# Performance work log

Hardware: AMD Instinct MI355X
Metric: run time of the kernel (lower is better)

## Reference

```python
import jax, jax.numpy as jnp
import numpy as np

NU, NM, D, E = 100000, 20000, 128, 1000000


def _seg_mean(feats, idx, n):
    # scatter-mean: zero for nodes with no incoming edges (PyG semantics)
    s = jax.ops.segment_sum(feats, idx, num_segments=n)
    c = jax.ops.segment_sum(jnp.ones((idx.shape[0], 1), feats.dtype), idx, num_segments=n)
    return s / jnp.maximum(c, 1.0)


def _hetero_sage(xu, xm, e_src, e_dst, Wl_um, Wr_um, b_um, Wl_mu, Wr_mu, b_mu):
    # ('user','rates','movie'): aggregate user features at movies
    agg_m = _seg_mean(xu[e_src], e_dst, xm.shape[0])          # [Nm, D]
    out_m = agg_m @ Wl_um + b_um + xm @ Wr_um                  # [Nm, H]
    # ('movie','rev_rates','user'): aggregate movie features at users
    agg_u = _seg_mean(xm[e_dst], e_src, xu.shape[0])          # [Nu, D]
    out_u = agg_u @ Wl_mu + b_mu + xu @ Wr_mu                  # [Nu, H]
    return out_u, out_m


def setup_inputs() -> dict:
    key = jax.random.key(0)
    ks = jax.random.split(key, 20)
    glorot = lambda k: (jax.random.normal(k, (D, D), jnp.float32) / np.sqrt(D)).astype(jnp.float32)
    inp = {
        "x_user": jax.random.normal(ks[0], (NU, D), jnp.float32),
        "x_movie": jax.random.normal(ks[1], (NM, D), jnp.float32),
        "edge_src": jax.random.randint(ks[2], (E,), 0, NU),
        "edge_dst": jax.random.randint(ks[3], (E,), 0, NM),
    }
    names = ["Wl1_um", "Wr1_um", "Wl1_mu", "Wr1_mu", "Wl2_um", "Wr2_um", "Wl2_mu", "Wr2_mu"]
    for i, n in enumerate(names):
        inp[n] = glorot(ks[4 + i])
    inp["b1_um"] = jnp.zeros((D,), jnp.float32)
    inp["b1_mu"] = jnp.zeros((D,), jnp.float32)
    inp["b2_um"] = jnp.zeros((D,), jnp.float32)
    inp["b2_mu"] = jnp.zeros((D,), jnp.float32)
    return inp


def reference(x_user, x_movie, Wl1_um, Wr1_um, Wl1_mu, Wr1_mu, Wl2_um, Wr2_um, Wl2_mu, Wr2_mu, b1_um, b1_mu, b2_um, b2_mu, edge_src, edge_dst):
    # layer 1 + relu (dropout = identity in eval) + residual
    h1_u, h1_m = _hetero_sage(x_user, x_movie, edge_src, edge_dst,
                              Wl1_um, Wr1_um, b1_um, Wl1_mu, Wr1_mu, b1_mu)
    r_u = x_user + jax.nn.relu(h1_u)
    r_m = x_movie + jax.nn.relu(h1_m)
    # layer 2 (dropout = identity in eval)
    out_u, out_m = _hetero_sage(r_u, r_m, edge_src, edge_dst,
                                Wl2_um, Wr2_um, b2_um, Wl2_mu, Wr2_mu, b2_mu)
    return out_u, out_m
```

## Files before the change

### kernel.cpp

```cpp
#include <hip/hip_runtime.h>
#include <stdint.h>

typedef unsigned short u16;
typedef unsigned int u32;
typedef __attribute__((ext_vector_type(8))) short short8;
typedef __attribute__((ext_vector_type(4))) float f32x4;
typedef __attribute__((ext_vector_type(4))) u32 u32x4;

__device__ __forceinline__ u16 f2bf(float f) {
    u32 x = __float_as_uint(f);
    u32 r = x + 0x7FFFu + ((x >> 16) & 1u);
    return (u16)(r >> 16);
}
__device__ __forceinline__ u32 pack2bf(float a, float b) {
    return (u32)f2bf(a) | ((u32)f2bf(b) << 16);
}
__device__ __forceinline__ float bflo(u32 w) { return __uint_as_float(w << 16); }
__device__ __forceinline__ float bfhi(u32 w) { return __uint_as_float(w & 0xFFFF0000u); }

struct WPtrs {
    const float* wl[4];
    const float* wr[4];
    u16* wout[4];
};

__global__ __launch_bounds__(256)
void prep_kernel(const int* __restrict__ src, const int* __restrict__ dst,
                 int* __restrict__ cnt, int* __restrict__ ranku,
                 int* __restrict__ rankm, int E, int nu, int nm,
                 const float* __restrict__ xu, const float* __restrict__ xm,
                 u32* __restrict__ xub, u32* __restrict__ xmb,
                 int eg4, int cg, WPtrs wp) {
    const int bid = blockIdx.x;
    const int tid = threadIdx.x;
    if (bid < eg4) {
        const int e0 = bid * 1024 + tid;
        int sv[4], dv[4];
        bool ok[4];
#pragma unroll
        for (int k = 0; k < 4; ++k) {
            int e = e0 + k * 256;
            ok[k] = (e < E);
            if (ok[k]) { sv[k] = src[e]; dv[k] = dst[e]; }
        }
#pragma unroll
        for (int k = 0; k < 4; ++k) {
            int e = e0 + k * 256;
            if (ok[k]) {
                if ((unsigned)sv[k] < (unsigned)nu &&
                    (unsigned)dv[k] < (unsigned)nm) {
                    ranku[e] = atomicAdd(&cnt[sv[k]], 1);
                    rankm[e] = atomicAdd(&cnt[nu + dv[k]], 1);
                } else {
                    ranku[e] = -1;
                }
            }
        }
    } else if (bid < eg4 + cg) {
        const int id = (bid - eg4) * 1024 + tid * 4;
        const int nuc = nu * 64;
        const int tot = nuc + nm * 64;
        if (id < tot) {
            const float* fin;
            u32* fout;
            int rel;
            if (id < nuc) { fin = xu; fout = xub; rel = id; }
            else          { fin = xm; fout = xmb; rel = id - nuc; }
            float4 p0 = ((const float4*)fin)[(rel >> 1)];
            float4 p1 = ((const float4*)fin)[(rel >> 1) + 1];
            u32x4 o = { pack2bf(p0.x, p0.y), pack2bf(p0.z, p0.w),
                        pack2bf(p1.x, p1.y), pack2bf(p1.z, p1.w) };
            *(u32x4*)(fout + rel) = o;
        }
    } else {
        const int unit = (bid - eg4 - cg) * 4 + (tid >> 6);
        if (unit < 256) {
            const int stack = unit >> 6, r = unit & 63, t = r >> 3, s = r & 7;
            const int lane = tid & 63;
            const float* Wl = wp.wl[stack];
            const float* Wr = wp.wr[stack];
            u16* outw = wp.wout[stack];
            const int n = t * 16 + (lane & 15);
            const int k0 = s * 32 + (lane >> 4) * 8;
            u16 v[8];
#pragma unroll
            for (int j = 0; j < 8; ++j) {
                int k = k0 + j;
                float f = (k < 128) ? Wl[k * 128 + n] : Wr[(k - 128) * 128 + n];
                v[j] = f2bf(f);
            }
            *(short8*)(outw + ((size_t)(t * 8 + s) * 64 + lane) * 8) = *(short8*)v;
        }
    }
}

__global__ __launch_bounds__(256)
void scan_partial(const int* __restrict__ cnt, int* __restrict__ bsum, int n) {
    __shared__ int s[256];
    const int tid = threadIdx.x;
    int base = blockIdx.x * 4096 + tid * 16;
    int sum = 0;
#pragma unroll
    for (int k = 0; k < 16; ++k) {
        int i = base + k;
        if (i < n) sum += cnt[i];
    }
    s[tid] = sum;
    __syncthreads();
    for (int d = 128; d > 0; d >>= 1) {
        if (tid < d) s[tid] += s[tid + d];
        __syncthreads();
    }
    if (tid == 0) bsum[blockIdx.x] = s[0];
}

__global__ __launch_bounds__(256)
void scan_apply(const int* __restrict__ cnt, const int* __restrict__ bsum,
                int* __restrict__ off, int n, int nb) {
    __shared__ int s[256];
    __shared__ int sb[64];
    __shared__ int pfx;
    const int tid = threadIdx.x;
    int base = blockIdx.x * 4096 + tid * 16;
    int v[16];
    int sum = 0;
#pragma unroll
    for (int k = 0; k < 16; ++k) {
        int i = base + k;
        v[k] = (i < n) ? cnt[i] : 0;
        sum += v[k];
    }
    s[tid] = sum;
    if (tid < 64) sb[tid] = (tid < nb) ? bsum[tid] : 0;
    __syncthreads();
    for (int d = 1; d < 256; d <<= 1) {
        int t = (tid >= d) ? s[tid - d] : 0;
        __syncthreads();
        s[tid] += t;
        __syncthreads();
    }
    if (tid == 0) {
        int p = 0;
        for (int b2 = 0; b2 < (int)blockIdx.x; ++b2) p += sb[b2];
        pfx = p;
        if ((int)blockIdx.x == nb - 1) off[n] = p + s[255];
    }
    __syncthreads();
    int run = pfx + s[tid] - sum;
#pragma unroll
    for (int k = 0; k < 16; ++k) {
        int i = base + k;
        if (i < n) off[i] = run;
        run += v[k];
    }
}

__global__ __launch_bounds__(256)
void fill_pos(const int* __restrict__ src, const int* __restrict__ dst,
              const int* __restrict__ ranku, const int* __restrict__ rankm,
              const int* __restrict__ off, int* __restrict__ nbr,
              int E, int nu) {
    const int e0 = blockIdx.x * 1024 + threadIdx.x;
    int sv[4], dv[4], ru[4], rm[4];
#pragma unroll
    for (int k = 0; k < 4; ++k) {
        int e = e0 + k * 256;
        ru[k] = -1;
        if (e < E) {
            ru[k] = ranku[e];
            sv[k] = src[e]; dv[k] = dst[e]; rm[k] = rankm[e];
        }
    }
#pragma unroll
    for (int k = 0; k < 4; ++k) {
        if (ru[k] >= 0) {
            nbr[off[sv[k]] + ru[k]] = dv[k];
            nbr[off[nu + dv[k]] + rm[k]] = sv[k];
        }
    }
}

template <int L1>
__device__ __forceinline__ void fused_body(
    const u32* __restrict__ featb, const float* __restrict__ xf,
    const u32* __restrict__ xb, const int* __restrict__ off,
    const int* __restrict__ nbr, const u16* __restrict__ wt,
    const float* __restrict__ bias, void* __restrict__ outp, int N, int blk) {
    __shared__ u32 sVb[16][132];
    const int tid = threadIdx.x;
    const int lane = tid & 63;
    const int wave = tid >> 6;
    const int base = blk * 16;
    const int q = lane >> 4;
    const int cl = lane & 15;

    for (int c = 0; c < 8; ++c) {
        const int i = wave * 8 + c;
        const int n = base + i;
        if (n < N) {
            const int b = off[n], e = off[n + 1];
            float a0 = 0.f, a1 = 0.f, a2 = 0.f, a3 = 0.f;
            float a4 = 0.f, a5 = 0.f, a6 = 0.f, a7 = 0.f;
            int t = b;
            for (; t + 15 < e; t += 16) {
                int g0 = nbr[t + q];
                int g1 = nbr[t + 4 + q];
                int g2 = nbr[t + 8 + q];
                int g3 = nbr[t + 12 + q];
                u32x4 v0 = *(const u32x4*)(featb + (size_t)g0 * 64 + cl * 4);
                u32x4 v1 = *(const u32x4*)(featb + (size_t)g1 * 64 + cl * 4);
                u32x4 v2 = *(const u32x4*)(featb + (size_t)g2 * 64 + cl * 4);
                u32x4 v3 = *(const u32x4*)(featb + (size_t)g3 * 64 + cl * 4);
                a0 += bflo(v0.x); a1 += bfhi(v0.x); a2 += bflo(v0.y); a3 += bfhi(v0.y);
                a4 += bflo(v0.z); a5 += bfhi(v0.z); a6 += bflo(v0.w); a7 += bfhi(v0.w);
                a0 += bflo(v1.x); a1 += bfhi(v1.x); a2 += bflo(v1.y); a3 += bfhi(v1.y);
                a4 += bflo(v1.z); a5 += bfhi(v1.z); a6 += bflo(v1.w); a7 += bfhi(v1.w);
                a0 += bflo(v2.x); a1 += bfhi(v2.x); a2 += bflo(v2.y); a3 += bfhi(v2.y);
                a4 += bflo(v2.z); a5 += bfhi(v2.z); a6 += bflo(v2.w); a7 += bfhi(v2.w);
                a0 += bflo(v3.x); a1 += bfhi(v3.x); a2 += bflo(v3.y); a3 += bfhi(v3.y);
                a4 += bflo(v3.z); a5 += bfhi(v3.z); a6 += bflo(v3.w); a7 += bfhi(v3.w);
            }
            for (; t < e; t += 4) {
                int it = t + q;
                if (it < e) {
                    u32x4 v = *(const u32x4*)(featb + (size_t)nbr[it] * 64 + cl * 4);
                    a0 += bflo(v.x); a1 += bfhi(v.x); a2 += bflo(v.y); a3 += bfhi(v.y);
                    a4 += bflo(v.z); a5 += bfhi(v.z); a6 += bflo(v.w); a7 += bfhi(v.w);
                }
            }
            a0 += __shfl_xor(a0, 16); a0 += __shfl_xor(a0, 32);
            a1 += __shfl_xor(a1, 16); a1 += __shfl_xor(a1, 32);
            a2 += __shfl_xor(a2, 16); a2 += __shfl_xor(a2, 32);
            a3 += __shfl_xor(a3, 16); a3 += __shfl_xor(a3, 32);
            a4 += __shfl_xor(a4, 16); a4 += __shfl_xor(a4, 32);
            a5 += __shfl_xor(a5, 16); a5 += __shfl_xor(a5, 32);
            a6 += __shfl_xor(a6, 16); a6 += __shfl_xor(a6, 32);
            a7 += __shfl_xor(a7, 16); a7 += __shfl_xor(a7, 32);
            const int dg = e - b;
            const float inv = 1.0f / (float)(dg > 1 ? dg : 1);
            if (q == 0) {
                u32x4 o = { pack2bf(a0 * inv, a1 * inv), pack2bf(a2 * inv, a3 * inv),
                            pack2bf(a4 * inv, a5 * inv), pack2bf(a6 * inv, a7 * inv) };
                *(u32x4*)&sVb[i][cl * 4] = o;
            }
            if (L1) {
                const float2 xv = ((const float2*)xf)[(size_t)n * 64 + lane];
                sVb[i][64 + lane] = pack2bf(xv.x, xv.y);
            } else {
                sVb[i][64 + lane] = xb[(size_t)n * 64 + lane];
            }
        } else {
            sVb[i][lane] = 0u;
            sVb[i][64 + lane] = 0u;
        }
    }
    __syncthreads();

    const int t0 = wave * 4;
    const u16* sVbu = (const u16*)sVb;
    const short8* wtp = (const short8*)wt;

    f32x4 acc0 = {0.f, 0.f, 0.f, 0.f};
    f32x4 acc1 = {0.f, 0.f, 0.f, 0.f};
    f32x4 acc2 = {0.f, 0.f, 0.f, 0.f};
    f32x4 acc3 = {0.f, 0.f, 0.f, 0.f};
#pragma unroll
    for (int s = 0; s < 8; ++s) {
        short8 a = *(const short8*)(sVbu + (size_t)cl * 264 + s * 32 + q * 8);
        short8 b0 = wtp[(size_t)((t0 + 0) * 8 + s) * 64 + lane];
        short8 b1 = wtp[(size_t)((t0 + 1) * 8 + s) * 64 + lane];
        short8 b2 = wtp[(size_t)((t0 + 2) * 8 + s) * 64 + lane];
        short8 b3 = wtp[(size_t)((t0 + 3) * 8 + s) * 64 + lane];
        acc0 = __builtin_amdgcn_mfma_f32_16x16x32_bf16(a, b0, acc0, 0, 0, 0);
        acc1 = __builtin_amdgcn_mfma_f32_16x16x32_bf16(a, b1, acc1, 0, 0, 0);
        acc2 = __builtin_amdgcn_mfma_f32_16x16x32_bf16(a, b2, acc2, 0, 0, 0);
        acc3 = __builtin_amdgcn_mfma_f32_16x16x32_bf16(a, b3, acc3, 0, 0, 0);
    }

#pragma unroll
    for (int tt = 0; tt < 4; ++tt) {
        const f32x4& cc = tt == 0 ? acc0 : tt == 1 ? acc1 : tt == 2 ? acc2 : acc3;
        const int nn = (t0 + tt) * 16 + cl;
        const float bj = bias[nn];
#pragma unroll
        for (int r = 0; r < 4; ++r) {
            const int m = q * 4 + r;
            const int node = base + m;
            if (node < N) {
                float h = cc[r] + bj;
                if (L1) {
                    u16* ob = (u16*)outp;
                    float x0 = xf[(size_t)node * 128 + nn];
                    ob[(size_t)node * 128 + nn] = f2bf(x0 + fmaxf(h, 0.f));
                } else {
                    float* o = (float*)outp;
                    o[(size_t)node * 128 + nn] = h;
                }
            }
        }
    }
}

__global__ __launch_bounds__(128, 8)
void fused_l1(const u32* __restrict__ featb, const float* __restrict__ xf,
              const int* __restrict__ off, const int* __restrict__ nbr,
              const u16* __restrict__ wt, const float* __restrict__ bias,
              void* __restrict__ outp, int N) {
    fused_body<1>(featb, xf, nullptr, off, nbr, wt, bias, outp, N, blockIdx.x);
}

__global__ __launch_bounds__(128, 8)
void fused_l2_dual(const u32* __restrict__ Abf, const u32* __restrict__ rmb,
                   const int* __restrict__ off, const int* __restrict__ nbr,
                   const u16* __restrict__ wtm, const u16* __restrict__ wtu,
                   const float* __restrict__ bm, const float* __restrict__ bu,
                   float* __restrict__ outm, float* __restrict__ outu,
                   int nm, int nu, int gm) {
    if ((int)blockIdx.x < gm)
        fused_body<0>(Abf, nullptr, rmb, off + nu, nbr, wtm, bm, outm, nm,
                      blockIdx.x);
    else
        fused_body<0>(rmb, nullptr, Abf, off, nbr, wtu, bu, outu, nu,
                      blockIdx.x - gm);
}

extern "C" void kernel_launch(void* const* d_in, const int* in_sizes, int n_in,
                              void* d_out, int out_size, void* d_ws, size_t ws_size,
                              hipStream_t stream) {
    const int nu = in_sizes[0] / 128;
    const int nm = in_sizes[1] / 128;
    const int E = in_sizes[2];

    const float* xu = (const float*)d_in[0];
    const float* xm = (const float*)d_in[1];
    const int* esrc = (const int*)d_in[2];
    const int* edst = (const int*)d_in[3];
    const float* Wl1_um = (const float*)d_in[4];
    const float* Wr1_um = (const float*)d_in[5];
    const float* Wl1_mu = (const float*)d_in[6];
    const float* Wr1_mu = (const float*)d_in[7];
    const float* Wl2_um = (const float*)d_in[8];
    const float* Wr2_um = (const float*)d_in[9];
    const float* Wl2_mu = (const float*)d_in[10];
    const float* Wr2_mu = (const float*)d_in[11];
    const float* b1_um = (const float*)d_in[12];
    const float* b1_mu = (const float*)d_in[13];
    const float* b2_um = (const float*)d_in[14];
    const float* b2_mu = (const float*)d_in[15];

    float* out_u = (float*)d_out;
    float* out_m = out_u + (size_t)nu * 128;

    const int ntot = nu + nm;
    const int NB = (ntot + 4095) / 4096;
    int* cnt = (int*)d_ws;
    int* off = cnt + ntot;
    int* bsum = off + ntot + 1;
    int* ranku = bsum + ((NB + 15) & ~15);
    int* rankm = ranku + E;
    int* nbr = rankm + E;
    size_t int_bytes = (size_t)((nbr + 2 * (size_t)E) - (int*)d_ws) * 4;
    size_t wt_off = (int_bytes + 63) & ~(size_t)63;
    u16* wt1_um = (u16*)((char*)d_ws + wt_off);
    u16* wt1_mu = wt1_um + 32768;
    u16* wt2_um = wt1_mu + 32768;
    u16* wt2_mu = wt2_um + 32768;
    u32* Abf = (u32*)((char*)d_ws + wt_off + 4 * 65536);
    u32* xmb = Abf + (size_t)nu * 64;
    u32* rmb = xmb + (size_t)nm * 64;

    const int eg4 = (E + 1023) / 1024;
    const int cg = ((nu + nm) * 64 + 1023) / 1024;

    WPtrs wp;
    wp.wl[0] = Wl1_um; wp.wr[0] = Wr1_um; wp.wout[0] = wt1_um;
    wp.wl[1] = Wl1_mu; wp.wr[1] = Wr1_mu; wp.wout[1] = wt1_mu;
    wp.wl[2] = Wl2_um; wp.wr[2] = Wr2_um; wp.wout[2] = wt2_um;
    wp.wl[3] = Wl2_mu; wp.wr[3] = Wr2_mu; wp.wout[3] = wt2_mu;

    hipMemsetAsync(cnt, 0, (size_t)ntot * 4, stream);
    prep_kernel<<<eg4 + cg + 64, 256, 0, stream>>>(
        esrc, edst, cnt, ranku, rankm, E, nu, nm, xu, xm, Abf, xmb, eg4, cg, wp);
    scan_partial<<<NB, 256, 0, stream>>>(cnt, bsum, ntot);
    scan_apply<<<NB, 256, 0, stream>>>(cnt, bsum, off, ntot, NB);
    fill_pos<<<eg4, 256, 0, stream>>>(esrc, edst, ranku, rankm, off, nbr, E, nu);

    const int gm = (nm + 15) / 16;
    const int gu = (nu + 15) / 16;

    fused_l1<<<gm, 128, 0, stream>>>(Abf, xm, off + nu, nbr, wt1_um, b1_um,
                                     rmb, nm);
    fused_l1<<<gu, 128, 0, stream>>>(xmb, xu, off, nbr, wt1_mu, b1_mu,
                                     Abf, nu);

    fused_l2_dual<<<gm + gu, 128, 0, stream>>>(
        Abf, rmb, off, nbr, wt2_um, wt2_mu, b2_um, b2_mu, out_m, out_u,
        nm, nu, gm);
}
```

Before: 513.9 us.

## Gather four destination nodes per wave concurrently instead of splitting edges across quarter-waves

The aggregation loop now assigns each quarter-wave (16 lanes) its own destination node, so a wave processes four nodes at once over two passes rather than one node at a time with edges split across quarters. This removes the cross-quarter shuffle reduction and the separate tail loop, and uses clamped indices with multiplicative masks to handle partial groups of four edges. The cost is divergence when the four nodes have different degrees, since the loop runs to the largest degree in the wave, plus some redundant masked loads. Out-of-range nodes now write zero aggregates through the same path because their degree is zero.

Measured after the change: 480.5 us. 6.5% less time.

```diff
diff --git a/kernel.cpp b/kernel.cpp
--- a/kernel.cpp
+++ b/kernel.cpp
@@ -194,55 +194,55 @@
     const int q = lane >> 4;
     const int cl = lane & 15;
 
+#pragma unroll
+    for (int gg = 0; gg < 2; ++gg) {
+        const int i = wave * 8 + gg * 4 + q;
+        const int n = base + i;
+        int b = 0, e2 = 0;
+        if (n < N) { b = off[n]; e2 = off[n + 1]; }
+        const int deg = e2 - b;
+        float a0 = 0.f, a1 = 0.f, a2 = 0.f, a3 = 0.f;
+        float a4 = 0.f, a5 = 0.f, a6 = 0.f, a7 = 0.f;
+        for (int j = 0; j < deg; j += 4) {
+            const int p = b + j;
+            const int p1 = (p + 1 < e2) ? p + 1 : e2 - 1;
+            const int p2 = (p + 2 < e2) ? p + 2 : e2 - 1;
+            const int p3 = (p + 3 < e2) ? p + 3 : e2 - 1;
+            const float m1 = (p + 1 < e2) ? 1.f : 0.f;
+            const float m2 = (p + 2 < e2) ? 1.f : 0.f;
+            const float m3 = (p + 3 < e2) ? 1.f : 0.f;
+            const int g0 = nbr[p];
+            const int g1 = nbr[p1];
+            const int g2 = nbr[p2];
+            const int g3 = nbr[p3];
+            u32x4 v0 = *(const u32x4*)(featb + (size_t)g0 * 64 + cl * 4);
+            u32x4 v1 = *(const u32x4*)(featb + (size_t)g1 * 64 + cl * 4);
+            u32x4 v2 = *(const u32x4*)(featb + (size_t)g2 * 64 + cl * 4);
+            u32x4 v3 = *(const u32x4*)(featb + (size_t)g3 * 64 + cl * 4);
+            a0 += bflo(v0.x); a1 += bfhi(v0.x); a2 += bflo(v0.y); a3 += bfhi(v0.y);
+            a4 += bflo(v0.z); a5 += bfhi(v0.z); a6 += bflo(v0.w); a7 += bfhi(v0.w);
+            a0 = fmaf(bflo(v1.x), m1, a0); a1 = fmaf(bfhi(v1.x), m1, a1);
+            a2 = fmaf(bflo(v1.y), m1, a2); a3 = fmaf(bfhi(v1.y), m1, a3);
+            a4 = fmaf(bflo(v1.z), m1, a4); a5 = fmaf(bfhi(v1.z), m1, a5);
+            a6 = fmaf(bflo(v1.w), m1, a6); a7 = fmaf(bfhi(v1.w), m1, a7);
+            a0 = fmaf(bflo(v2.x), m2, a0); a1 = fmaf(bfhi(v2.x), m2, a1);
+            a2 = fmaf(bflo(v2.y), m2, a2); a3 = fmaf(bfhi(v2.y), m2, a3);
+            a4 = fmaf(bflo(v2.z), m2, a4); a5 = fmaf(bfhi(v2.z), m2, a5);
+            a6 = fmaf(bflo(v2.w), m2, a6); a7 = fmaf(bfhi(v2.w), m2, a7);
+            a0 = fmaf(bflo(v3.x), m3, a0); a1 = fmaf(bfhi(v3.x), m3, a1);
+            a2 = fmaf(bflo(v3.y), m3, a2); a3 = fmaf(bfhi(v3.y), m3, a3);
+            a4 = fmaf(bflo(v3.z), m3, a4); a5 = fmaf(bfhi(v3.z), m3, a5);
+            a6 = fmaf(bflo(v3.w), m3, a6); a7 = fmaf(bfhi(v3.w), m3, a7);
+        }
+        const float inv = 1.0f / (float)(deg > 1 ? deg : 1);
+        u32x4 o = { pack2bf(a0 * inv, a1 * inv), pack2bf(a2 * inv, a3 * inv),
+                    pack2bf(a4 * inv, a5 * inv), pack2bf(a6 * inv, a7 * inv) };
+        *(u32x4*)&sVb[i][cl * 4] = o;
+    }
     for (int c = 0; c < 8; ++c) {
         const int i = wave * 8 + c;
         const int n = base + i;
         if (n < N) {
-            const int b = off[n], e = off[n + 1];
-            float a0 = 0.f, a1 = 0.f, a2 = 0.f, a3 = 0.f;
-            float a4 = 0.f, a5 = 0.f, a6 = 0.f, a7 = 0.f;
-            int t = b;
-            for (; t + 15 < e; t += 16) {
-                int g0 = nbr[t + q];
-                int g1 = nbr[t + 4 + q];
-                int g2 = nbr[t + 8 + q];
-                int g3 = nbr[t + 12 + q];
-                u32x4 v0 = *(const u32x4*)(featb + (size_t)g0 * 64 + cl * 4);
-                u32x4 v1 = *(const u32x4*)(featb + (size_t)g1 * 64 + cl * 4);
-                u32x4 v2 = *(const u32x4*)(featb + (size_t)g2 * 64 + cl * 4);
-                u32x4 v3 = *(const u32x4*)(featb + (size_t)g3 * 64 + cl * 4);
-                a0 += bflo(v0.x); a1 += bfhi(v0.x); a2 += bflo(v0.y); a3 += bfhi(v0.y);
-                a4 += bflo(v0.z); a5 += bfhi(v0.z); a6 += bflo(v0.w); a7 += bfhi(v0.w);
-                a0 += bflo(v1.x); a1 += bfhi(v1.x); a2 += bflo(v1.y); a3 += bfhi(v1.y);
-                a4 += bflo(v1.z); a5 += bfhi(v1.z); a6 += bflo(v1.w); a7 += bfhi(v1.w);
-                a0 += bflo(v2.x); a1 += bfhi(v2.x); a2 += bflo(v2.y); a3 += bfhi(v2.y);
-                a4 += bflo(v2.z); a5 += bfhi(v2.z); a6 += bflo(v2.w); a7 += bfhi(v2.w);
-                a0 += bflo(v3.x); a1 += bfhi(v3.x); a2 += bflo(v3.y); a3 += bfhi(v3.y);
-                a4 += bflo(v3.z); a5 += bfhi(v3.z); a6 += bflo(v3.w); a7 += bfhi(v3.w);
-            }
-            for (; t < e; t += 4) {
-                int it = t + q;
-                if (it < e) {
-                    u32x4 v = *(const u32x4*)(featb + (size_t)nbr[it] * 64 + cl * 4);
-                    a0 += bflo(v.x); a1 += bfhi(v.x); a2 += bflo(v.y); a3 += bfhi(v.y);
-                    a4 += bflo(v.z); a5 += bfhi(v.z); a6 += bflo(v.w); a7 += bfhi(v.w);
-                }
-            }
-            a0 += __shfl_xor(a0, 16); a0 += __shfl_xor(a0, 32);
-            a1 += __shfl_xor(a1, 16); a1 += __shfl_xor(a1, 32);
-            a2 += __shfl_xor(a2, 16); a2 += __shfl_xor(a2, 32);
-            a3 += __shfl_xor(a3, 16); a3 += __shfl_xor(a3, 32);
-            a4 += __shfl_xor(a4, 16); a4 += __shfl_xor(a4, 32);
-            a5 += __shfl_xor(a5, 16); a5 += __shfl_xor(a5, 32);
-            a6 += __shfl_xor(a6, 16); a6 += __shfl_xor(a6, 32);
-            a7 += __shfl_xor(a7, 16); a7 += __shfl_xor(a7, 32);
-            const int dg = e - b;
-            const float inv = 1.0f / (float)(dg > 1 ? dg : 1);
-            if (q == 0) {
-                u32x4 o = { pack2bf(a0 * inv, a1 * inv), pack2bf(a2 * inv, a3 * inv),
-                            pack2bf(a4 * inv, a5 * inv), pack2bf(a6 * inv, a7 * inv) };
-                *(u32x4*)&sVb[i][cl * 4] = o;
-            }
             if (L1) {
                 const float2 xv = ((const float2*)xf)[(size_t)n * 64 + lane];
                 sVb[i][64 + lane] = pack2bf(xv.x, xv.y);
@@ -250,7 +250,6 @@
                 sVb[i][64 + lane] = xb[(size_t)n * 64 + lane];
             }
         } else {
-            sVb[i][lane] = 0u;
             sVb[i][64 + lane] = 0u;
         }
     }
```
